# Optimization experiments

Measured on AMD Instinct MI355X. Metric: run time of the kernel, lower is better.

Reference implementation:

```python
import jax, jax.numpy as jnp
import numpy as np

EMBED_DIM = 1024
NUM_HEADS = 16
BLOCK_SIZE = 128
GLOBAL_EVERY = 24


def make_block_sparse_mask(seq_len):
    # 0 where allowed, -inf where disallowed. Allowed iff same block, or
    # either position lies in a 'global' block (block index % global_every == 0).
    bi = jnp.arange(seq_len) // BLOCK_SIZE
    is_global = (bi % GLOBAL_EVERY) == 0
    allowed = (bi[:, None] == bi[None, :]) | is_global[:, None] | is_global[None, :]
    return jnp.where(allowed, 0.0, -jnp.inf).astype(jnp.float32)


def setup_inputs() -> dict:
    key = jax.random.key(0)
    k_x, k_w, k_wo = jax.random.split(key, 3)
    B, L, D = 1, 4096, EMBED_DIM
    x = jax.random.normal(k_x, (B, L, D), dtype=jnp.float32)
    # nn.MultiheadAttention params: packed in_proj [3D, D] + bias [3D], out_proj [D, D] + bias [D]
    w_qkv = jax.random.normal(k_w, (3 * D, D), dtype=jnp.float32) * 0.02
    b_qkv = jnp.zeros((3 * D,), dtype=jnp.float32)
    w_out = jax.random.normal(k_wo, (D, D), dtype=jnp.float32) * 0.02
    b_out = jnp.zeros((D,), dtype=jnp.float32)
    return {"x": x, "w_qkv": w_qkv, "b_qkv": b_qkv, "w_out": w_out, "b_out": b_out}


def reference(x, w_qkv, b_qkv, w_out, b_out):
    B, L, D = x.shape
    H = NUM_HEADS
    hd = D // H
    mask = make_block_sparse_mask(L)  # [L, L] additive
    qkv = x @ w_qkv.T + b_qkv  # [B, L, 3D]
    q, k, v = jnp.split(qkv, 3, axis=-1)
    # [B, H, L, hd]
    q = q.reshape(B, L, H, hd).transpose(0, 2, 1, 3)
    k = k.reshape(B, L, H, hd).transpose(0, 2, 1, 3)
    v = v.reshape(B, L, H, hd).transpose(0, 2, 1, 3)
    scale = 1.0 / jnp.sqrt(jnp.asarray(hd, dtype=x.dtype))
    scores = jnp.einsum('bhqd,bhkd->bhqk', q * scale, k) + mask  # [B, H, L, L]
    attn = jax.nn.softmax(scores, axis=-1)
    out = jnp.einsum('bhqk,bhkd->bhqd', attn, v)  # [B, H, L, hd]
    out = out.transpose(0, 2, 1, 3).reshape(B, L, D)
    return out @ w_out.T + b_out
```

## Files before the change

### kernel.cpp

```cpp
#include <hip/hip_runtime.h>
#include <hip/hip_bf16.h>
#include <math.h>


#define SEQ 4096
#define DIM 1024
#define NHEADS 16
#define HDIM 64
#define BS 128
#define ESTRIDE 136

using short8 = __attribute__((ext_vector_type(8))) short;
using floatx4 = __attribute__((ext_vector_type(4))) float;

__device__ __forceinline__ float bf2f(short s) {
  unsigned u = ((unsigned)(unsigned short)s) << 16;
  return __uint_as_float(u);
}

__device__ __forceinline__ unsigned pack_bf16(float a, float b) {
  __hip_bfloat16 ba = __float2bfloat16(a);
  __hip_bfloat16 bb = __float2bfloat16(b);
  return ((unsigned)*(unsigned short*)&bb << 16) | (unsigned)*(unsigned short*)&ba;
}

__device__ __forceinline__ void gld_lds16(const __hip_bfloat16* g, __hip_bfloat16* l) {
  __builtin_amdgcn_global_load_lds(
      (const __attribute__((address_space(1))) unsigned int*)g,
      (__attribute__((address_space(3))) unsigned int*)l, 16, 0, 0);
}

__global__ __launch_bounds__(256) void downcast3(
    const float* __restrict__ x, const float* __restrict__ wq,
    const float* __restrict__ wo, __hip_bfloat16* __restrict__ xd,
    __hip_bfloat16* __restrict__ wqd, __hip_bfloat16* __restrict__ wod) {
  int id = blockIdx.x;
  const float* src;
  __hip_bfloat16* dst;
  int base;
  if (id < 4096) { src = x; dst = xd; base = id; }
  else if (id < 7168) { src = wq; dst = wqd; base = id - 4096; }
  else { src = wo; dst = wod; base = id - 7168; }
  int i = (base * 256 + threadIdx.x) * 4;
  float4 v = *(const float4*)(src + i);
  __hip_bfloat16 b0 = __float2bfloat16(v.x);
  __hip_bfloat16 b1 = __float2bfloat16(v.y);
  __hip_bfloat16 b2 = __float2bfloat16(v.z);
  __hip_bfloat16 b3 = __float2bfloat16(v.w);
  ushort4 packed = {*(unsigned short*)&b0, *(unsigned short*)&b1,
                    *(unsigned short*)&b2, *(unsigned short*)&b3};
  *(ushort4*)(((unsigned short*)dst) + i) = packed;
}

__global__ __launch_bounds__(256) void gemm_qkv(const __hip_bfloat16* __restrict__ Amat,
                                                const __hip_bfloat16* __restrict__ Wmat,
                                                const float* __restrict__ Bias,
                                                __hip_bfloat16* __restrict__ qkv) {
  __shared__ __align__(16) char pool[128 * ESTRIDE * 2];
  __hip_bfloat16* Asmem = (__hip_bfloat16*)pool;
  __hip_bfloat16* Bsmem = (__hip_bfloat16*)(pool + 8192);
  __hip_bfloat16* Ep = (__hip_bfloat16*)pool;

  const int Kd = DIM;
  const int t = threadIdx.x;
  const int w = t >> 6;
  const int lane = t & 63;
  const int fr = lane & 15;
  const int quad = lane >> 4;
  const int wm = w >> 1, wn = w & 1;

  int id = blockIdx.x;
  int xcd = id & 7, j = id >> 3;
  int m_idx = xcd + (j & 3) * 8;
  int n_idx = j >> 2;
  const int m0 = m_idx * 128;
  const int n0 = n_idx * 128;
  const int s = n0 >> 10;
  const int cc0 = n0 & 1023;
  const bool vmode = (s == 2);

  const __hip_bfloat16* APtr = vmode ? Amat + (size_t)m0 * Kd : Wmat + (size_t)n0 * Kd;
  const __hip_bfloat16* BPtr = vmode ? Wmat + (size_t)n0 * Kd : Amat + (size_t)m0 * Kd;

  floatx4 acc[4][4];
#pragma unroll
  for (int i = 0; i < 4; ++i)
#pragma unroll
    for (int jj = 0; jj < 4; ++jj) acc[i][jj] = (floatx4){0.f, 0.f, 0.f, 0.f};

  for (int kk = 0; kk < Kd / 32; ++kk) {
#pragma unroll
    for (int jj = 0; jj < 2; ++jj) {
      int c = jj * 256 + t;
      int ldso = (jj * 256 + w * 64) * 8;
      gld_lds16(APtr + (size_t)(c >> 2) * Kd + kk * 32 + (c & 3) * 8, &Asmem[ldso]);
      gld_lds16(BPtr + (size_t)(c >> 2) * Kd + kk * 32 + (c & 3) * 8, &Bsmem[ldso]);
    }
    __syncthreads();
    short8 af[4], bf_[4];
#pragma unroll
    for (int mt = 0; mt < 4; ++mt)
      af[mt] = *(const short8*)&Asmem[(wm * 64 + mt * 16 + fr) * 32 + quad * 8];
#pragma unroll
    for (int nt = 0; nt < 4; ++nt)
      bf_[nt] = *(const short8*)&Bsmem[(wn * 64 + nt * 16 + fr) * 32 + quad * 8];
#pragma unroll
    for (int mt = 0; mt < 4; ++mt)
#pragma unroll
      for (int nt = 0; nt < 4; ++nt)
        acc[mt][nt] = __builtin_amdgcn_mfma_f32_16x16x32_bf16(af[mt], bf_[nt],
                                                              acc[mt][nt], 0, 0, 0);
    __syncthreads();
  }

#pragma unroll
  for (int nt = 0; nt < 4; ++nt) {
    int dcol = wn * 64 + nt * 16 + fr;
#pragma unroll
    for (int mt = 0; mt < 4; ++mt) {
      int drow0 = wm * 64 + mt * 16 + quad * 4;
      ushort4 pk;
      unsigned short* pks = (unsigned short*)&pk;
#pragma unroll
      for (int i = 0; i < 4; ++i) {
        __hip_bfloat16 bb = __float2bfloat16(acc[mt][nt][i]);
        pks[i] = *(unsigned short*)&bb;
      }
      *(ushort4*)&Ep[dcol * ESTRIDE + drow0] = pk;
    }
  }
  __syncthreads();

  if (!vmode) {
    __hip_bfloat16* dst = qkv + (size_t)s * SEQ * DIM;
#pragma unroll
    for (int rr = 0; rr < 8; ++rr) {
      int m = rr * 16 + (t >> 4);
      int ch = (t & 15) * 8;
      short8 v8 = *(const short8*)&Ep[m * ESTRIDE + ch];
      float4 b0 = *(const float4*)&Bias[n0 + ch];
      float4 b1 = *(const float4*)&Bias[n0 + ch + 4];
      float bb[8] = {b0.x, b0.y, b0.z, b0.w, b1.x, b1.y, b1.z, b1.w};
      short8 o8;
#pragma unroll
      for (int k = 0; k < 8; ++k) {
        __hip_bfloat16 ob = __float2bfloat16(bf2f(v8[k]) + bb[k]);
        o8[k] = *(short*)&ob;
      }
      *(short8*)&dst[(size_t)(m0 + m) * DIM + cc0 + ch] = o8;
    }
  } else {
    __hip_bfloat16* vt = qkv + 2ull * SEQ * DIM;
#pragma unroll
    for (int rr = 0; rr < 8; ++rr) {
      int nrow = rr * 16 + (t >> 4);
      int ch = (t & 15) * 8;
      float bv = Bias[n0 + nrow];
      short8 v8 = *(const short8*)&Ep[nrow * ESTRIDE + ch];
      short8 o8;
#pragma unroll
      for (int k = 0; k < 8; ++k) {
        __hip_bfloat16 ob = __float2bfloat16(bf2f(v8[k]) + bv);
        o8[k] = *(short*)&ob;
      }
      *(short8*)&vt[(size_t)(cc0 + nrow) * SEQ + m0 + ch] = o8;
    }
  }
}

__global__ __launch_bounds__(256) void gemm_out(const __hip_bfloat16* __restrict__ Amat,
                                                const __hip_bfloat16* __restrict__ Wmat,
                                                const float* __restrict__ Bias,
                                                float* __restrict__ out) {
  __shared__ __align__(16) __hip_bfloat16 Asmem[128 * 32];
  __shared__ __align__(16) __hip_bfloat16 Bsmem[64 * 32];
  const int Kd = DIM;
  const int t = threadIdx.x;
  const int w = t >> 6;
  const int lane = t & 63;
  const int fr = lane & 15;
  const int quad = lane >> 4;
  const int wm = w >> 1, wn = w & 1;
  int id = blockIdx.x;
  int xcd = id & 7, j = id >> 3;
  int m_idx = xcd + (j & 3) * 8;
  int n_idx = j >> 2;
  const int m0 = m_idx * 128;
  const int n0 = n_idx * 64;
  const __hip_bfloat16* Ablk = Amat + (size_t)m0 * Kd;
  const __hip_bfloat16* Bblk = Wmat + (size_t)n0 * Kd;
  floatx4 acc[4][2];
#pragma unroll
  for (int i = 0; i < 4; ++i)
#pragma unroll
    for (int jj = 0; jj < 2; ++jj) acc[i][jj] = (floatx4){0.f, 0.f, 0.f, 0.f};
  for (int kk = 0; kk < Kd / 32; ++kk) {
#pragma unroll
    for (int jj = 0; jj < 2; ++jj) {
      int c = jj * 256 + t;
      int ldso = (jj * 256 + w * 64) * 8;
      gld_lds16(Ablk + (size_t)(c >> 2) * Kd + kk * 32 + (c & 3) * 8, &Asmem[ldso]);
    }
    gld_lds16(Bblk + (size_t)(t >> 2) * Kd + kk * 32 + (t & 3) * 8, &Bsmem[t * 8]);
    __syncthreads();
    short8 af[4], bf_[2];
#pragma unroll
    for (int mt = 0; mt < 4; ++mt)
      af[mt] = *(const short8*)&Asmem[(wm * 64 + mt * 16 + fr) * 32 + quad * 8];
#pragma unroll
    for (int nt = 0; nt < 2; ++nt)
      bf_[nt] = *(const short8*)&Bsmem[(wn * 32 + nt * 16 + fr) * 32 + quad * 8];
#pragma unroll
    for (int mt = 0; mt < 4; ++mt)
#pragma unroll
      for (int nt = 0; nt < 2; ++nt)
        acc[mt][nt] = __builtin_amdgcn_mfma_f32_16x16x32_bf16(af[mt], bf_[nt],
                                                              acc[mt][nt], 0, 0, 0);
    __syncthreads();
  }
#pragma unroll
  for (int nt = 0; nt < 2; ++nt) {
    int n = n0 + wn * 32 + nt * 16 + fr;
    float bv = Bias[n];
#pragma unroll
    for (int mt = 0; mt < 4; ++mt) {
      int m = m0 + wm * 64 + mt * 16 + quad * 4;
#pragma unroll
      for (int i = 0; i < 4; ++i)
        out[(size_t)(m + i) * DIM + n] = acc[mt][nt][i] + bv;
    }
  }
}

__global__ __launch_bounds__(256) void attn_mfma(
    const __hip_bfloat16* __restrict__ qkv,
    __hip_bfloat16* __restrict__ aout,
    float* __restrict__ po, float* __restrict__ pm, float* __restrict__ pl) {
  __shared__ __align__(16) __hip_bfloat16 Kbuf[16 * 512];
  __shared__ __align__(16) __hip_bfloat16 Vbuf[16 * 512];
  const int h = blockIdx.y;
  const int wgid = blockIdx.x;
  const int t = threadIdx.x;
  const int wv = t >> 6;
  const int lane = t & 63;
  const int fr = lane & 15;
  const int quad = lane >> 4;

  int qb, niter, slice = 0, pid = 0;
  bool direct;
  if (wgid < 30) {
    qb = (wgid < 23) ? wgid + 1 : wgid + 2;
    niter = 3;
    direct = true;
  } else {
    int gi = wgid - 30;
    slice = gi & 7;
    int qc = gi >> 3;
    qb = qc * 24;
    niter = 4;
    direct = false;
    pid = (h * 2 + qc) * 8 + slice;
  }
  const int q0 = qb * BS;

  const __hip_bfloat16* Q = qkv;
  const __hip_bfloat16* K = qkv + (size_t)SEQ * DIM;
  const __hip_bfloat16* Vt = qkv + 2ull * SEQ * DIM;

  short8 qaA0, qaA1, qaB0, qaB1;
  {
    const __hip_bfloat16* qp =
        Q + (size_t)(q0 + wv * 16 + fr) * DIM + h * HDIM + quad * 8;
    qaA0 = *(const short8*)(qp);
    qaA1 = *(const short8*)(qp + 32);
    qp += (size_t)64 * DIM;
    qaB0 = *(const short8*)(qp);
    qaB1 = *(const short8*)(qp + 32);
  }

  float mA = -INFINITY, lA = 0.f, mB = -INFINITY, lB = 0.f;
  floatx4 oA[4], oB[4];
#pragma unroll
  for (int i = 0; i < 4; ++i) {
    oA[i] = (floatx4){0.f, 0.f, 0.f, 0.f};
    oB[i] = (floatx4){0.f, 0.f, 0.f, 0.f};
  }

  for (int bi = 0; bi < niter; ++bi) {
    int kb = direct ? (bi == 0 ? 0 : (bi == 1 ? qb : 24)) : slice * 4 + bi;

    const __hip_bfloat16* Kg = K + (size_t)(kb * BS) * DIM + h * HDIM;
    const __hip_bfloat16* Vg = Vt + (size_t)(h * HDIM) * SEQ + kb * BS;
    __syncthreads();
#pragma unroll
    for (int rr = 0; rr < 4; ++rr) {
      int f = rr * 4 + wv;
      int nt = f >> 1, ks = f & 1;
      gld_lds16(Kg + (size_t)(nt * 16 + fr) * DIM + ks * 32 + quad * 8,
                &Kbuf[f * 512]);
      int nt2 = f >> 2, ks2 = f & 3;
      gld_lds16(Vg + (size_t)(nt2 * 16 + fr) * SEQ + ks2 * 32 + quad * 8,
                &Vbuf[f * 512]);
    }
    __syncthreads();

#pragma unroll
    for (int rg = 0; rg < 2; ++rg) {
      short8 q0f = rg ? qaB0 : qaA0;
      short8 q1f = rg ? qaB1 : qaA1;
      float mrow = rg ? mB : mA;
      float lsum = rg ? lB : lA;

      floatx4 s[8];
#pragma unroll
      for (int nt = 0; nt < 8; ++nt) {
        short8 kf0 = *(const short8*)&Kbuf[(nt * 2 + 0) * 512 + lane * 8];
        short8 kf1 = *(const short8*)&Kbuf[(nt * 2 + 1) * 512 + lane * 8];
        floatx4 acc = {0.f, 0.f, 0.f, 0.f};
        acc = __builtin_amdgcn_mfma_f32_16x16x32_bf16(kf0, q0f, acc, 0, 0, 0);
        acc = __builtin_amdgcn_mfma_f32_16x16x32_bf16(kf1, q1f, acc, 0, 0, 0);
        s[nt] = acc;
      }
#pragma unroll
      for (int nt = 0; nt < 8; ++nt)
#pragma unroll
        for (int i = 0; i < 4; ++i) s[nt][i] *= 0.125f;

      float rmax = -INFINITY;
#pragma unroll
      for (int nt = 0; nt < 8; ++nt)
#pragma unroll
        for (int i = 0; i < 4; ++i) rmax = fmaxf(rmax, s[nt][i]);
      rmax = fmaxf(rmax, __shfl_xor(rmax, 16, 64));
      rmax = fmaxf(rmax, __shfl_xor(rmax, 32, 64));
      float newm = fmaxf(mrow, rmax);
      float alpha = __expf(mrow - newm);
      float psum = 0.f;
      unsigned pki[8][2];
#pragma unroll
      for (int nt = 0; nt < 8; ++nt) {
        float p0 = __expf(s[nt][0] - newm);
        float p1 = __expf(s[nt][1] - newm);
        float p2 = __expf(s[nt][2] - newm);
        float p3 = __expf(s[nt][3] - newm);
        psum += (p0 + p1) + (p2 + p3);
        pki[nt][0] = pack_bf16(p0, p1);
        pki[nt][1] = pack_bf16(p2, p3);
      }
      psum += __shfl_xor(psum, 16, 64);
      psum += __shfl_xor(psum, 32, 64);
      lsum = lsum * alpha + psum;
      mrow = newm;
      if (rg) { mB = mrow; lB = lsum; } else { mA = mrow; lA = lsum; }

#pragma unroll
      for (int nt2 = 0; nt2 < 4; ++nt2)
#pragma unroll
        for (int i = 0; i < 4; ++i) {
          if (rg) oB[nt2][i] *= alpha; else oA[nt2][i] *= alpha;
        }

#pragma unroll
      for (int ks2 = 0; ks2 < 4; ++ks2) {
        union { int w4[4]; short8 s8; } pw;
#pragma unroll
        for (int p = 0; p < 4; ++p) {
          int srcl = fr + ((((quad & 1) << 1) + (p >> 1)) << 4);
          int lo = __shfl((int)pki[2 * ks2][p & 1], srcl, 64);
          int hi = __shfl((int)pki[2 * ks2 + 1][p & 1], srcl, 64);
          pw.w4[p] = (quad & 2) ? hi : lo;
        }
#pragma unroll
        for (int nt2 = 0; nt2 < 4; ++nt2) {
          short8 vb = *(const short8*)&Vbuf[(nt2 * 4 + ks2) * 512 + lane * 8];
          if (rg)
            oB[nt2] = __builtin_amdgcn_mfma_f32_16x16x32_bf16(vb, pw.s8, oB[nt2], 0, 0, 0);
          else
            oA[nt2] = __builtin_amdgcn_mfma_f32_16x16x32_bf16(vb, pw.s8, oA[nt2], 0, 0, 0);
        }
      }
    }
  }

  if (direct) {
#pragma unroll
    for (int rg = 0; rg < 2; ++rg) {
      float inv = 1.f / (rg ? lB : lA);
      __hip_bfloat16* orow = aout +
          (size_t)(q0 + rg * 64 + wv * 16 + fr) * DIM + h * HDIM + quad * 4;
#pragma unroll
      for (int nt2 = 0; nt2 < 4; ++nt2) {
        ushort4 pk;
        unsigned short* pks = (unsigned short*)&pk;
#pragma unroll
        for (int i = 0; i < 4; ++i) {
          float ov = rg ? oB[nt2][i] : oA[nt2][i];
          __hip_bfloat16 ob = __float2bfloat16(ov * inv);
          pks[i] = *(unsigned short*)&ob;
        }
        *(ushort4*)(orow + nt2 * 16) = pk;
      }
    }
  } else {
#pragma unroll
    for (int rg = 0; rg < 2; ++rg) {
      float* pob = po + (size_t)pid * 8192 + (rg * 64 + wv * 16 + fr) * 64 + quad * 4;
#pragma unroll
      for (int nt2 = 0; nt2 < 4; ++nt2) {
        floatx4 ov = rg ? oB[nt2] : oA[nt2];
        float4 v = {ov[0], ov[1], ov[2], ov[3]};
        *(float4*)(pob + nt2 * 16) = v;
      }
      if (quad == 0) {
        pm[pid * 128 + rg * 64 + wv * 16 + fr] = rg ? mB : mA;
        pl[pid * 128 + rg * 64 + wv * 16 + fr] = rg ? lB : lA;
      }
    }
  }
}

__global__ __launch_bounds__(256) void combine(const float* __restrict__ po,
                                               const float* __restrict__ pm,
                                               const float* __restrict__ pl,
                                               __hip_bfloat16* __restrict__ aout) {
  int b2 = blockIdx.x;
  int h = b2 >> 2, qc = (b2 >> 1) & 1, half = b2 & 1;
  int bb = h * 2 + qc;
  int t = threadIdx.x;
  int row = half * 64 + (t >> 2);
  int d0 = (t & 3) * 16;

  float m8[8];
  float newm = -INFINITY;
#pragma unroll
  for (int s = 0; s < 8; ++s) {
    m8[s] = pm[(bb * 8 + s) * 128 + row];
    newm = fmaxf(newm, m8[s]);
  }
  float wgt[8], lsum = 0.f;
#pragma unroll
  for (int s = 0; s < 8; ++s) {
    wgt[s] = __expf(m8[s] - newm);
    lsum += pl[(bb * 8 + s) * 128 + row] * wgt[s];
  }
  float acc[16];
#pragma unroll
  for (int jj = 0; jj < 16; ++jj) acc[jj] = 0.f;
#pragma unroll
  for (int s = 0; s < 8; ++s) {
    const float* src = po + ((size_t)(bb * 8 + s) * 8192) + row * 64 + d0;
#pragma unroll
    for (int j4 = 0; j4 < 4; ++j4) {
      float4 v = *(const float4*)(src + j4 * 4);
      acc[j4 * 4 + 0] += wgt[s] * v.x;
      acc[j4 * 4 + 1] += wgt[s] * v.y;
      acc[j4 * 4 + 2] += wgt[s] * v.z;
      acc[j4 * 4 + 3] += wgt[s] * v.w;
    }
  }
  float inv = 1.f / lsum;
  int qrow = qc * 3072 + row;
#pragma unroll
  for (int jj = 0; jj < 16; ++jj)
    aout[(size_t)qrow * DIM + h * HDIM + d0 + jj] = __float2bfloat16(acc[jj] * inv);
}

extern "C" void kernel_launch(void* const* d_in, const int* in_sizes, int n_in,
                              void* d_out, int out_size, void* d_ws, size_t ws_size,
                              hipStream_t stream) {
  const float* x = (const float*)d_in[0];
  const float* w_qkv = (const float*)d_in[1];
  const float* b_qkv = (const float*)d_in[2];
  const float* w_out = (const float*)d_in[3];
  const float* b_out = (const float*)d_in[4];
  float* out = (float*)d_out;

  char* wsb = (char*)d_ws;
  __hip_bfloat16* qkv_ws = (__hip_bfloat16*)(wsb);
  __hip_bfloat16* x_bf = (__hip_bfloat16*)(wsb + 24ull * 1024 * 1024);
  __hip_bfloat16* wqkv_bf = (__hip_bfloat16*)(wsb + 32ull * 1024 * 1024);
  __hip_bfloat16* wout_bf = (__hip_bfloat16*)(wsb + 38ull * 1024 * 1024);
  __hip_bfloat16* attn_ws = (__hip_bfloat16*)(wsb + 40ull * 1024 * 1024);
  float* po = (float*)(wsb + 24ull * 1024 * 1024);
  float* pm = (float*)(wsb + 32ull * 1024 * 1024);
  float* pl = (float*)(wsb + 32ull * 1024 * 1024 + 131072);

  dim3 blk(256);
  downcast3<<<dim3(8192), blk, 0, stream>>>(x, w_qkv, w_out, x_bf, wqkv_bf, wout_bf);
  gemm_qkv<<<dim3(768), blk, 0, stream>>>(x_bf, wqkv_bf, b_qkv, qkv_ws);
  attn_mfma<<<dim3(46, NHEADS), blk, 0, stream>>>(qkv_ws, attn_ws, po, pm, pl);
  combine<<<dim3(64), blk, 0, stream>>>(po, pm, pl, attn_ws);
  gemm_out<<<dim3(512), blk, 0, stream>>>(attn_ws, wout_bf, b_out, out);
}
```

Baseline: 178.5 us.

## Double K-tile depth in both GEMMs and interleave two row groups in attention

Both projection GEMMs now load 64-wide K slices per iteration instead of 32. Each barrier pair therefore covers twice the MFMA work and the loop runs half as many iterations. The attention inner loop now processes the two 64-row groups together instead of one after another. This shares K/V fragment loads and exposes independent MFMA and exp chains for latency hiding. It costs more LDS and more live registers, which could lower occupancy or cause spills.

```diff
diff --git a/kernel.cpp b/kernel.cpp
--- a/kernel.cpp
+++ b/kernel.cpp
@@ -58,7 +58,7 @@
                                                 __hip_bfloat16* __restrict__ qkv) {
   __shared__ __align__(16) char pool[128 * ESTRIDE * 2];
   __hip_bfloat16* Asmem = (__hip_bfloat16*)pool;
-  __hip_bfloat16* Bsmem = (__hip_bfloat16*)(pool + 8192);
+  __hip_bfloat16* Bsmem = (__hip_bfloat16*)(pool + 16384);
   __hip_bfloat16* Ep = (__hip_bfloat16*)pool;
 
   const int Kd = DIM;
@@ -88,28 +88,37 @@
 #pragma unroll
     for (int jj = 0; jj < 4; ++jj) acc[i][jj] = (floatx4){0.f, 0.f, 0.f, 0.f};
 
-  for (int kk = 0; kk < Kd / 32; ++kk) {
-#pragma unroll
-    for (int jj = 0; jj < 2; ++jj) {
+  for (int kk = 0; kk < Kd / 64; ++kk) {
+#pragma unroll
+    for (int jj = 0; jj < 4; ++jj) {
       int c = jj * 256 + t;
       int ldso = (jj * 256 + w * 64) * 8;
-      gld_lds16(APtr + (size_t)(c >> 2) * Kd + kk * 32 + (c & 3) * 8, &Asmem[ldso]);
-      gld_lds16(BPtr + (size_t)(c >> 2) * Kd + kk * 32 + (c & 3) * 8, &Bsmem[ldso]);
+      int row = (c & 511) >> 2;
+      int col = ((c >> 9) << 5) + ((c & 3) << 3);
+      gld_lds16(APtr + (size_t)row * Kd + kk * 64 + col, &Asmem[ldso]);
+      gld_lds16(BPtr + (size_t)row * Kd + kk * 64 + col, &Bsmem[ldso]);
     }
     __syncthreads();
-    short8 af[4], bf_[4];
+    short8 af[4][2], bf_[4][2];
 #pragma unroll
     for (int mt = 0; mt < 4; ++mt)
-      af[mt] = *(const short8*)&Asmem[(wm * 64 + mt * 16 + fr) * 32 + quad * 8];
+#pragma unroll
+      for (int ks = 0; ks < 2; ++ks)
+        af[mt][ks] = *(const short8*)&Asmem[ks * 4096 + (wm * 64 + mt * 16 + fr) * 32 + quad * 8];
 #pragma unroll
     for (int nt = 0; nt < 4; ++nt)
-      bf_[nt] = *(const short8*)&Bsmem[(wn * 64 + nt * 16 + fr) * 32 + quad * 8];
+#pragma unroll
+      for (int ks = 0; ks < 2; ++ks)
+        bf_[nt][ks] = *(const short8*)&Bsmem[ks * 4096 + (wn * 64 + nt * 16 + fr) * 32 + quad * 8];
 #pragma unroll
     for (int mt = 0; mt < 4; ++mt)
 #pragma unroll
-      for (int nt = 0; nt < 4; ++nt)
-        acc[mt][nt] = __builtin_amdgcn_mfma_f32_16x16x32_bf16(af[mt], bf_[nt],
+      for (int nt = 0; nt < 4; ++nt) {
+        acc[mt][nt] = __builtin_amdgcn_mfma_f32_16x16x32_bf16(af[mt][0], bf_[nt][0],
                                                               acc[mt][nt], 0, 0, 0);
+        acc[mt][nt] = __builtin_amdgcn_mfma_f32_16x16x32_bf16(af[mt][1], bf_[nt][1],
+                                                              acc[mt][nt], 0, 0, 0);
+      }
     __syncthreads();
   }
 
@@ -172,8 +181,8 @@
                                                 const __hip_bfloat16* __restrict__ Wmat,
                                                 const float* __restrict__ Bias,
                                                 float* __restrict__ out) {
-  __shared__ __align__(16) __hip_bfloat16 Asmem[128 * 32];
-  __shared__ __align__(16) __hip_bfloat16 Bsmem[64 * 32];
+  __shared__ __align__(16) __hip_bfloat16 Asmem[128 * 64];
+  __shared__ __align__(16) __hip_bfloat16 Bsmem[64 * 64];
   const int Kd = DIM;
   const int t = threadIdx.x;
   const int w = t >> 6;
@@ -194,28 +203,44 @@
   for (int i = 0; i < 4; ++i)
 #pragma unroll
     for (int jj = 0; jj < 2; ++jj) acc[i][jj] = (floatx4){0.f, 0.f, 0.f, 0.f};
-  for (int kk = 0; kk < Kd / 32; ++kk) {
+  for (int kk = 0; kk < Kd / 64; ++kk) {
+#pragma unroll
+    for (int jj = 0; jj < 4; ++jj) {
+      int c = jj * 256 + t;
+      int ldso = (jj * 256 + w * 64) * 8;
+      int row = (c & 511) >> 2;
+      int col = ((c >> 9) << 5) + ((c & 3) << 3);
+      gld_lds16(Ablk + (size_t)row * Kd + kk * 64 + col, &Asmem[ldso]);
+    }
 #pragma unroll
     for (int jj = 0; jj < 2; ++jj) {
       int c = jj * 256 + t;
       int ldso = (jj * 256 + w * 64) * 8;
-      gld_lds16(Ablk + (size_t)(c >> 2) * Kd + kk * 32 + (c & 3) * 8, &Asmem[ldso]);
-    }
-    gld_lds16(Bblk + (size_t)(t >> 2) * Kd + kk * 32 + (t & 3) * 8, &Bsmem[t * 8]);
+      int row = (c & 255) >> 2;
+      int col = ((c >> 8) << 5) + ((c & 3) << 3);
+      gld_lds16(Bblk + (size_t)row * Kd + kk * 64 + col, &Bsmem[ldso]);
+    }
     __syncthreads();
-    short8 af[4], bf_[2];
+    short8 af[4][2], bf_[2][2];
 #pragma unroll
     for (int mt = 0; mt < 4; ++mt)
-      af[mt] = *(const short8*)&Asmem[(wm * 64 + mt * 16 + fr) * 32 + quad * 8];
+#pragma unroll
+      for (int ks = 0; ks < 2; ++ks)
+        af[mt][ks] = *(const short8*)&Asmem[ks * 4096 + (wm * 64 + mt * 16 + fr) * 32 + quad * 8];
 #pragma unroll
     for (int nt = 0; nt < 2; ++nt)
-      bf_[nt] = *(const short8*)&Bsmem[(wn * 32 + nt * 16 + fr) * 32 + quad * 8];
+#pragma unroll
+      for (int ks = 0; ks < 2; ++ks)
+        bf_[nt][ks] = *(const short8*)&Bsmem[ks * 2048 + (wn * 32 + nt * 16 + fr) * 32 + quad * 8];
 #pragma unroll
     for (int mt = 0; mt < 4; ++mt)
 #pragma unroll
-      for (int nt = 0; nt < 2; ++nt)
-        acc[mt][nt] = __builtin_amdgcn_mfma_f32_16x16x32_bf16(af[mt], bf_[nt],
+      for (int nt = 0; nt < 2; ++nt) {
+        acc[mt][nt] = __builtin_amdgcn_mfma_f32_16x16x32_bf16(af[mt][0], bf_[nt][0],
                                                               acc[mt][nt], 0, 0, 0);
+        acc[mt][nt] = __builtin_amdgcn_mfma_f32_16x16x32_bf16(af[mt][1], bf_[nt][1],
+                                                              acc[mt][nt], 0, 0, 0);
+      }
     __syncthreads();
   }
 #pragma unroll
@@ -304,80 +329,95 @@
     }
     __syncthreads();
 
-#pragma unroll
-    for (int rg = 0; rg < 2; ++rg) {
-      short8 q0f = rg ? qaB0 : qaA0;
-      short8 q1f = rg ? qaB1 : qaA1;
-      float mrow = rg ? mB : mA;
-      float lsum = rg ? lB : lA;
-
-      floatx4 s[8];
-#pragma unroll
-      for (int nt = 0; nt < 8; ++nt) {
-        short8 kf0 = *(const short8*)&Kbuf[(nt * 2 + 0) * 512 + lane * 8];
-        short8 kf1 = *(const short8*)&Kbuf[(nt * 2 + 1) * 512 + lane * 8];
-        floatx4 acc = {0.f, 0.f, 0.f, 0.f};
-        acc = __builtin_amdgcn_mfma_f32_16x16x32_bf16(kf0, q0f, acc, 0, 0, 0);
-        acc = __builtin_amdgcn_mfma_f32_16x16x32_bf16(kf1, q1f, acc, 0, 0, 0);
-        s[nt] = acc;
-      }
-#pragma unroll
-      for (int nt = 0; nt < 8; ++nt)
-#pragma unroll
-        for (int i = 0; i < 4; ++i) s[nt][i] *= 0.125f;
-
-      float rmax = -INFINITY;
-#pragma unroll
-      for (int nt = 0; nt < 8; ++nt)
-#pragma unroll
-        for (int i = 0; i < 4; ++i) rmax = fmaxf(rmax, s[nt][i]);
-      rmax = fmaxf(rmax, __shfl_xor(rmax, 16, 64));
-      rmax = fmaxf(rmax, __shfl_xor(rmax, 32, 64));
-      float newm = fmaxf(mrow, rmax);
-      float alpha = __expf(mrow - newm);
-      float psum = 0.f;
-      unsigned pki[8][2];
-#pragma unroll
-      for (int nt = 0; nt < 8; ++nt) {
-        float p0 = __expf(s[nt][0] - newm);
-        float p1 = __expf(s[nt][1] - newm);
-        float p2 = __expf(s[nt][2] - newm);
-        float p3 = __expf(s[nt][3] - newm);
-        psum += (p0 + p1) + (p2 + p3);
-        pki[nt][0] = pack_bf16(p0, p1);
-        pki[nt][1] = pack_bf16(p2, p3);
-      }
-      psum += __shfl_xor(psum, 16, 64);
-      psum += __shfl_xor(psum, 32, 64);
-      lsum = lsum * alpha + psum;
-      mrow = newm;
-      if (rg) { mB = mrow; lB = lsum; } else { mA = mrow; lA = lsum; }
-
-#pragma unroll
-      for (int nt2 = 0; nt2 < 4; ++nt2)
-#pragma unroll
-        for (int i = 0; i < 4; ++i) {
-          if (rg) oB[nt2][i] *= alpha; else oA[nt2][i] *= alpha;
-        }
-
-#pragma unroll
-      for (int ks2 = 0; ks2 < 4; ++ks2) {
-        union { int w4[4]; short8 s8; } pw;
-#pragma unroll
-        for (int p = 0; p < 4; ++p) {
-          int srcl = fr + ((((quad & 1) << 1) + (p >> 1)) << 4);
-          int lo = __shfl((int)pki[2 * ks2][p & 1], srcl, 64);
-          int hi = __shfl((int)pki[2 * ks2 + 1][p & 1], srcl, 64);
-          pw.w4[p] = (quad & 2) ? hi : lo;
-        }
-#pragma unroll
-        for (int nt2 = 0; nt2 < 4; ++nt2) {
-          short8 vb = *(const short8*)&Vbuf[(nt2 * 4 + ks2) * 512 + lane * 8];
-          if (rg)
-            oB[nt2] = __builtin_amdgcn_mfma_f32_16x16x32_bf16(vb, pw.s8, oB[nt2], 0, 0, 0);
-          else
-            oA[nt2] = __builtin_amdgcn_mfma_f32_16x16x32_bf16(vb, pw.s8, oA[nt2], 0, 0, 0);
-        }
+    floatx4 sA[8], sB[8];
+#pragma unroll
+    for (int nt = 0; nt < 8; ++nt) {
+      short8 kf0 = *(const short8*)&Kbuf[(nt * 2 + 0) * 512 + lane * 8];
+      short8 kf1 = *(const short8*)&Kbuf[(nt * 2 + 1) * 512 + lane * 8];
+      floatx4 a = {0.f, 0.f, 0.f, 0.f};
+      floatx4 b = {0.f, 0.f, 0.f, 0.f};
+      a = __builtin_amdgcn_mfma_f32_16x16x32_bf16(kf0, qaA0, a, 0, 0, 0);
+      b = __builtin_amdgcn_mfma_f32_16x16x32_bf16(kf0, qaB0, b, 0, 0, 0);
+      a = __builtin_amdgcn_mfma_f32_16x16x32_bf16(kf1, qaA1, a, 0, 0, 0);
+      b = __builtin_amdgcn_mfma_f32_16x16x32_bf16(kf1, qaB1, b, 0, 0, 0);
+      sA[nt] = a;
+      sB[nt] = b;
+    }
+#pragma unroll
+    for (int nt = 0; nt < 8; ++nt)
+#pragma unroll
+      for (int i = 0; i < 4; ++i) {
+        sA[nt][i] *= 0.125f;
+        sB[nt][i] *= 0.125f;
+      }
+
+    float rA = -INFINITY, rB = -INFINITY;
+#pragma unroll
+    for (int nt = 0; nt < 8; ++nt)
+#pragma unroll
+      for (int i = 0; i < 4; ++i) {
+        rA = fmaxf(rA, sA[nt][i]);
+        rB = fmaxf(rB, sB[nt][i]);
+      }
+    rA = fmaxf(rA, __shfl_xor(rA, 16, 64));
+    rB = fmaxf(rB, __shfl_xor(rB, 16, 64));
+    rA = fmaxf(rA, __shfl_xor(rA, 32, 64));
+    rB = fmaxf(rB, __shfl_xor(rB, 32, 64));
+    float newmA = fmaxf(mA, rA), newmB = fmaxf(mB, rB);
+    float alphaA = __expf(mA - newmA), alphaB = __expf(mB - newmB);
+    float psA = 0.f, psB = 0.f;
+    unsigned pkiA[8][2], pkiB[8][2];
+#pragma unroll
+    for (int nt = 0; nt < 8; ++nt) {
+      float a0 = __expf(sA[nt][0] - newmA);
+      float a1 = __expf(sA[nt][1] - newmA);
+      float a2 = __expf(sA[nt][2] - newmA);
+      float a3 = __expf(sA[nt][3] - newmA);
+      psA += (a0 + a1) + (a2 + a3);
+      pkiA[nt][0] = pack_bf16(a0, a1);
+      pkiA[nt][1] = pack_bf16(a2, a3);
+      float b0 = __expf(sB[nt][0] - newmB);
+      float b1 = __expf(sB[nt][1] - newmB);
+      float b2 = __expf(sB[nt][2] - newmB);
+      float b3 = __expf(sB[nt][3] - newmB);
+      psB += (b0 + b1) + (b2 + b3);
+      pkiB[nt][0] = pack_bf16(b0, b1);
+      pkiB[nt][1] = pack_bf16(b2, b3);
+    }
+    psA += __shfl_xor(psA, 16, 64);
+    psB += __shfl_xor(psB, 16, 64);
+    psA += __shfl_xor(psA, 32, 64);
+    psB += __shfl_xor(psB, 32, 64);
+    lA = lA * alphaA + psA;
+    lB = lB * alphaB + psB;
+    mA = newmA;
+    mB = newmB;
+#pragma unroll
+    for (int nt2 = 0; nt2 < 4; ++nt2)
+#pragma unroll
+      for (int i = 0; i < 4; ++i) {
+        oA[nt2][i] *= alphaA;
+        oB[nt2][i] *= alphaB;
+      }
+
+#pragma unroll
+    for (int ks2 = 0; ks2 < 4; ++ks2) {
+      union { int w4[4]; short8 s8; } pwA, pwB;
+#pragma unroll
+      for (int p = 0; p < 4; ++p) {
+        int srcl = fr + ((((quad & 1) << 1) + (p >> 1)) << 4);
+        int loA = __shfl((int)pkiA[2 * ks2][p & 1], srcl, 64);
+        int hiA = __shfl((int)pkiA[2 * ks2 + 1][p & 1], srcl, 64);
+        pwA.w4[p] = (quad & 2) ? hiA : loA;
+        int loB = __shfl((int)pkiB[2 * ks2][p & 1], srcl, 64);
+        int hiB = __shfl((int)pkiB[2 * ks2 + 1][p & 1], srcl, 64);
+        pwB.w4[p] = (quad & 2) ? hiB : loB;
+      }
+#pragma unroll
+      for (int nt2 = 0; nt2 < 4; ++nt2) {
+        short8 vb = *(const short8*)&Vbuf[(nt2 * 4 + ks2) * 512 + lane * 8];
+        oA[nt2] = __builtin_amdgcn_mfma_f32_16x16x32_bf16(vb, pwA.s8, oA[nt2], 0, 0, 0);
+        oB[nt2] = __builtin_amdgcn_mfma_f32_16x16x32_bf16(vb, pwB.s8, oB[nt2], 0, 0, 0);
       }
     }
   }
```

Result: slower. 190.9 us (+7.0%).
